# Kernel tuning notes

Hardware: AMD Instinct MI355X
Metric: run time of the kernel (lower is better)

The kernel has to match this reference:

```python
import jax, jax.numpy as jnp
import numpy as np

N_NODES = 100000

def gcn_conv(x, edge_index, W, b, n_nodes):
    # GCNConv: out = D^{-1/2} (A + I) D^{-1/2} X W + b  (self-loops added)
    src, dst = edge_index[0], edge_index[1]
    loops = jnp.arange(n_nodes, dtype=edge_index.dtype)
    src = jnp.concatenate([src, loops])
    dst = jnp.concatenate([dst, loops])
    deg = jax.ops.segment_sum(jnp.ones_like(dst, dtype=x.dtype), dst, num_segments=n_nodes)
    dinv = jnp.where(deg > 0, jax.lax.rsqrt(deg), 0.0)
    norm = dinv[src] * dinv[dst]  # [E+N]
    h = x @ W  # transform first (small d), then gather/scatter
    msgs = h[src] * norm[:, None]
    out = jax.ops.segment_sum(msgs, dst, num_segments=n_nodes)
    return out + b


def setup_inputs() -> dict:
    key = jax.random.key(0)
    k1, k2, k3, k4, k5, k6 = jax.random.split(key, 6)
    x = jax.random.normal(k1, (N_NODES, 3), dtype=jnp.float32)
    edge_index = jax.random.randint(k2, (2, 2400000), 0, N_NODES, dtype=jnp.int64)
    # Glorot-style init for GCNConv linear weights; zero bias matches PyG default
    W1 = jax.random.normal(k3, (3, 16), dtype=jnp.float32) * (1.0 / np.sqrt(3))
    b1 = jnp.zeros((16,), dtype=jnp.float32)
    W2 = jax.random.normal(k4, (16, 32), dtype=jnp.float32) * (1.0 / np.sqrt(16))
    b2 = jnp.zeros((32,), dtype=jnp.float32)
    return {"x": x, "edge_index": edge_index, "W1": W1, "b1": b1, "W2": W2, "b2": b2}


def reference(x, edge_index, W1, b1, W2, b2):
    n = x.shape[0]
    h = gcn_conv(x, edge_index, W1, b1, n)
    h = jax.nn.relu(h)
    h = gcn_conv(h, edge_index, W2, b2, n)
    # batch is all zeros in the original forward -> single-graph mean pool
    return jnp.mean(h, axis=0, keepdims=True)  # [1, 32]
```

## Files before the change

kernel.cpp:

```cpp
#include <hip/hip_runtime.h>

typedef unsigned int uint;
typedef unsigned long long ull;


#define MAXB  256
#define CAP   16384u
#define BINB  512
#define CHUNK 4096
#define AFS   2048.0f
#define AFB   16384
#define AFM   0x1FFFFFu
#define PADN  131072

__global__ void __launch_bounds__(BINB)
bin2_kernel(const int* __restrict__ srcI, const int* __restrict__ dstI,
            uint* __restrict__ curDg, uint* __restrict__ curSg,
            uint* __restrict__ bufD, uint* __restrict__ bufS, int E) {
    __shared__ uint cntD[MAXB], scanD[MAXB], baseD[MAXB];
    __shared__ uint cntS[MAXB], scanS[MAXB], baseS[MAXB];
    __shared__ uint stageD[CHUNK];
    __shared__ uint stageS[CHUNK];
    const int tid = threadIdx.x;
    const int e0 = blockIdx.x * CHUNK;
    const int nE = min(CHUNK, E - e0);
    const int my0 = tid * 8;
    const int myc = max(0, min(8, nE - my0));
    if (tid < MAXB) cntD[tid] = 0u; else cntS[tid - MAXB] = 0u;

    uint d8[8], s8[8], rD[8], rS[8];
    if (myc == 8) {
        int4 ka = ((const int4*)(dstI + e0))[tid * 2];
        int4 kb = ((const int4*)(dstI + e0))[tid * 2 + 1];
        int4 oa = ((const int4*)(srcI + e0))[tid * 2];
        int4 ob = ((const int4*)(srcI + e0))[tid * 2 + 1];
        d8[0] = ka.x; d8[1] = ka.y; d8[2] = ka.z; d8[3] = ka.w;
        d8[4] = kb.x; d8[5] = kb.y; d8[6] = kb.z; d8[7] = kb.w;
        s8[0] = oa.x; s8[1] = oa.y; s8[2] = oa.z; s8[3] = oa.w;
        s8[4] = ob.x; s8[5] = ob.y; s8[6] = ob.z; s8[7] = ob.w;
    } else {
        for (int r = 0; r < myc; ++r) {
            d8[r] = (uint)dstI[e0 + my0 + r];
            s8[r] = (uint)srcI[e0 + my0 + r];
        }
    }
    __syncthreads();
    for (int r = 0; r < myc; ++r) {
        rD[r] = atomicAdd(&cntD[d8[r] >> 9], 1u);
        rS[r] = atomicAdd(&cntS[s8[r] >> 9], 1u);
    }
    __syncthreads();
    const int half = tid >> 8;
    const int li = tid & 255;
    uint* cn = half ? cntS : cntD;
    uint* sc = half ? scanS : scanD;
    sc[li] = cn[li];
    __syncthreads();
    for (int d = 1; d < MAXB; d <<= 1) {
        uint t = (li >= d) ? sc[li - d] : 0u;
        __syncthreads();
        sc[li] += t;
        __syncthreads();
    }
    {
        uint* cur = half ? curSg : curDg;
        uint* bs = half ? baseS : baseD;
        bs[li] = (uint)li * CAP + (cn[li] ? atomicAdd(&cur[li * 16], cn[li]) : 0u);
    }
    __syncthreads();
    for (int r = 0; r < myc; ++r) {
        uint bD = d8[r] >> 9;
        stageD[(scanD[bD] - cntD[bD]) + rD[r]] = ((d8[r] & 511u) << 17) | s8[r];
        uint bS = s8[r] >> 9;
        stageS[(scanS[bS] - cntS[bS]) + rS[r]] = ((s8[r] & 511u) << 17) | d8[r];
    }
    __syncthreads();
    const int wave = tid >> 6, lane = tid & 63;
    if (wave < 4) {
        for (int b = wave; b < MAXB; b += 4) {
            uint s0 = scanD[b] - cntD[b], c = cntD[b], gb = baseD[b];
            uint lim = (uint)(b + 1) * CAP;
            for (uint i = lane; i < c; i += 64u) {
                uint gp = gb + i;
                if (gp < lim) bufD[gp] = stageD[s0 + i];
            }
        }
    } else {
        for (int b = wave - 4; b < MAXB; b += 4) {
            uint s0 = scanS[b] - cntS[b], c = cntS[b], gb = baseS[b];
            uint lim = (uint)(b + 1) * CAP;
            for (uint i = lane; i < c; i += 64u) {
                uint gp = gb + i;
                if (gp < lim) bufS[gp] = stageS[s0 + i];
            }
        }
    }
}

__global__ void __launch_bounds__(1024)
degnode_kernel(const uint* __restrict__ buf, const uint* __restrict__ curD,
               const float* __restrict__ x, uint* __restrict__ degg,
               float* __restrict__ dinv, float4* __restrict__ xd4, int n) {
    __shared__ uint dg[512];
    const int tid = threadIdx.x;
    const int b = blockIdx.x;
    const uint base = (uint)b * CAP;
    const uint c = min(curD[b * 16], CAP);
    if (tid < 512) dg[tid] = 0u;
    __syncthreads();
    for (uint i0 = (uint)tid * 8u; i0 < c; i0 += 8192u) {
        uint cnt8 = min(8u, c - i0);
        uint en[8];
        if (cnt8 == 8u) {
            uint4 a = ((const uint4*)(buf + base + i0))[0];
            uint4 bb = ((const uint4*)(buf + base + i0))[1];
            en[0] = a.x; en[1] = a.y; en[2] = a.z; en[3] = a.w;
            en[4] = bb.x; en[5] = bb.y; en[6] = bb.z; en[7] = bb.w;
        } else {
            for (uint r = 0; r < cnt8; ++r) en[r] = buf[base + i0 + r];
        }
        for (uint r = 0; r < cnt8; ++r) atomicAdd(&dg[en[r] >> 17], 1u);
    }
    __syncthreads();
    if (tid < 512) {
        int node = (b << 9) + tid;
        if (node < n) {
            uint d = dg[tid];
            degg[node] = d;
            float di = rsqrtf((float)(d + 1u));
            dinv[node] = di;
            xd4[node] = make_float4(x[3 * node] * di, x[3 * node + 1] * di,
                                    x[3 * node + 2] * di, di);
        }
    }
}

__global__ void __launch_bounds__(1024)
aggqT_kernel(const uint* __restrict__ bufD, const uint* __restrict__ curD,
             const uint* __restrict__ bufS, const uint* __restrict__ curS,
             const uint* __restrict__ degg, const float* __restrict__ dinv,
             const float4* __restrict__ xd4, const float* __restrict__ W1,
             const float* __restrict__ b1, float* __restrict__ T, int n) {
    __shared__ ull acc[512];
    __shared__ float gl[512];
    __shared__ float taccs[16];
    const int tid = threadIdx.x;
    const int b = blockIdx.x;
    const uint base = (uint)b * CAP;
    const uint cD = min(curD[b * 16], CAP);
    const uint cS = min(curS[b * 16], CAP);
    if (tid < 512) { acc[tid] = 0ull; gl[tid] = 0.0f; }
    if (tid < 16) taccs[tid] = 0.0f;
    __syncthreads();
    for (uint i0 = (uint)tid * 8u; i0 < cS; i0 += 8192u) {
        uint cnt8 = min(8u, cS - i0);
        uint en[8];
        if (cnt8 == 8u) {
            uint4 a = ((const uint4*)(bufS + base + i0))[0];
            uint4 bb = ((const uint4*)(bufS + base + i0))[1];
            en[0] = a.x; en[1] = a.y; en[2] = a.z; en[3] = a.w;
            en[4] = bb.x; en[5] = bb.y; en[6] = bb.z; en[7] = bb.w;
        } else {
            for (uint r = 0; r < cnt8; ++r) en[r] = bufS[base + i0 + r];
            for (uint r = cnt8; r < 8u; ++r) en[r] = en[0];
        }
        float dv[8];
#pragma unroll
        for (int r = 0; r < 8; ++r) dv[r] = dinv[en[r] & 0x1FFFFu];
#pragma unroll
        for (uint r = 0; r < 8u; ++r)
            if (r < cnt8) atomicAdd(&gl[en[r] >> 17], dv[r]);
    }
    for (uint i0 = (uint)tid * 8u; i0 < cD; i0 += 8192u) {
        uint cnt8 = min(8u, cD - i0);
        uint en[8];
        if (cnt8 == 8u) {
            uint4 a = ((const uint4*)(bufD + base + i0))[0];
            uint4 bb = ((const uint4*)(bufD + base + i0))[1];
            en[0] = a.x; en[1] = a.y; en[2] = a.z; en[3] = a.w;
            en[4] = bb.x; en[5] = bb.y; en[6] = bb.z; en[7] = bb.w;
        } else {
            for (uint r = 0; r < cnt8; ++r) en[r] = bufD[base + i0 + r];
            for (uint r = cnt8; r < 8u; ++r) en[r] = en[0];
        }
        float4 gv[8];
#pragma unroll
        for (int r = 0; r < 8; ++r) gv[r] = xd4[en[r] & 0x1FFFFu];
#pragma unroll
        for (uint r = 0; r < 8u; ++r) {
            if (r < cnt8) {
                uint dl = en[r] >> 17;
                ull f0 = (ull)(uint)((int)rintf(gv[r].x * AFS) + AFB);
                ull f1 = (ull)(uint)((int)rintf(gv[r].y * AFS) + AFB);
                ull f2 = (ull)(uint)((int)rintf(gv[r].z * AFS) + AFB);
                atomicAdd(&acc[dl], f0 | (f1 << 21) | (f2 << 42));
            }
        }
    }
    __syncthreads();
    float sq[16];
#pragma unroll
    for (int k = 0; k < 16; ++k) sq[k] = 0.0f;
    if (tid < 512) {
        int node = (b << 9) + tid;
        if (node < n) {
            ull v = acc[tid];
            int ub = (int)(degg[node] * (uint)AFB);
            float4 sv = xd4[node];
            float di = sv.w;
            const float isc = 1.0f / AFS;
            float av = (float)((int)(uint)(v & AFM) - ub) * isc + sv.x;
            float bv = (float)((int)(uint)((v >> 21) & AFM) - ub) * isc + sv.y;
            float cv = (float)((int)(uint)((v >> 42) & AFM) - ub) * isc + sv.z;
            float w = gl[tid] + di;
#pragma unroll
            for (int k = 0; k < 16; ++k) {
                float h = di * (av * W1[k] + bv * W1[16 + k] + cv * W1[32 + k]) + b1[k];
                h = fmaxf(h, 0.0f);
                sq[k] = w * (di * h);
            }
        }
    }
#pragma unroll
    for (int k = 0; k < 16; ++k) {
        float v2 = sq[k];
        for (int off = 32; off > 0; off >>= 1) v2 += __shfl_down(v2, off, 64);
        if ((tid & 63) == 0) atomicAdd(&taccs[k], v2);
    }
    __syncthreads();
    if (tid < 16 && taccs[tid] != 0.0f) atomicAdd(&T[tid], taccs[tid]);
}

__global__ void out_kernel(const float* __restrict__ T, const float* __restrict__ W2,
                           const float* __restrict__ b2, float* __restrict__ out, float invN) {
    int j = threadIdx.x;
    float s = 0.0f;
#pragma unroll
    for (int k = 0; k < 16; ++k) s += T[k] * W2[k * 32 + j];
    out[j] = b2[j] + invN * s;
}

extern "C" void kernel_launch(void* const* d_in, const int* in_sizes, int n_in,
                              void* d_out, int out_size, void* d_ws, size_t ws_size,
                              hipStream_t stream) {
    const float* x   = (const float*)d_in[0];
    const int*   ei  = (const int*)d_in[1];
    const float* W1  = (const float*)d_in[2];
    const float* b1  = (const float*)d_in[3];
    const float* W2  = (const float*)d_in[4];
    const float* b2  = (const float*)d_in[5];
    float* out = (float*)d_out;

    const int n = in_sizes[0] / 3;
    const int E = in_sizes[1] / 2;
    const int* src = ei;
    const int* dst = ei + E;

    char* p = (char*)d_ws;
    float* T    = (float*)p;    p += 64;
    uint*  curD = (uint*)p;     p += MAXB * 16 * 4;
    uint*  curS = (uint*)p;     p += MAXB * 16 * 4;
    size_t zbytes = (size_t)(p - (char*)d_ws);
    uint*  degg  = (uint*)p;    p += (size_t)n * 4;
    float* dinv  = (float*)p;   p += (size_t)n * 4;
    uint*  bufD  = (uint*)p;    p += (size_t)MAXB * CAP * 4;
    uint*  bufS  = (uint*)p;    p += (size_t)MAXB * CAP * 4;
    p = (char*)(((size_t)p + 31) & ~(size_t)31);
    float4* xd4  = (float4*)p;  p += (size_t)PADN * 16;

    const int nb = (n + 511) >> 9;

    hipMemsetAsync(d_ws, 0, zbytes, stream);
    bin2_kernel<<<(E + CHUNK - 1) / CHUNK, BINB, 0, stream>>>(src, dst, curD, curS, bufD, bufS, E);
    degnode_kernel<<<nb, 1024, 0, stream>>>(bufD, curD, x, degg, dinv, xd4, n);
    aggqT_kernel<<<nb, 1024, 0, stream>>>(bufD, curD, bufS, curS, degg, dinv, xd4, W1, b1, T, n);
    out_kernel<<<1, 32, 0, stream>>>(T, W2, b2, out, 1.0f / (float)n);
}
```

Measured before the change: 144.6 us.

## Flatten bin scatter, split aggregation sweeps across half-blocks, fuse output via last-block

```diff
diff --git a/kernel.cpp b/kernel.cpp
--- a/kernel.cpp
+++ b/kernel.cpp
@@ -2,6 +2,7 @@
 
 typedef unsigned int uint;
 typedef unsigned long long ull;
+typedef unsigned char uchar;
 
 
 #define MAXB  256
@@ -17,10 +18,12 @@
 bin2_kernel(const int* __restrict__ srcI, const int* __restrict__ dstI,
             uint* __restrict__ curDg, uint* __restrict__ curSg,
             uint* __restrict__ bufD, uint* __restrict__ bufS, int E) {
-    __shared__ uint cntD[MAXB], scanD[MAXB], baseD[MAXB];
-    __shared__ uint cntS[MAXB], scanS[MAXB], baseS[MAXB];
+    __shared__ uint cntD[MAXB], scanD[MAXB], deltaD[MAXB];
+    __shared__ uint cntS[MAXB], scanS[MAXB], deltaS[MAXB];
     __shared__ uint stageD[CHUNK];
     __shared__ uint stageS[CHUNK];
+    __shared__ uchar stBD[CHUNK];
+    __shared__ uchar stBS[CHUNK];
     const int tid = threadIdx.x;
     const int e0 = blockIdx.x * CHUNK;
     const int nE = min(CHUNK, E - e0);
@@ -64,35 +67,32 @@
     }
     {
         uint* cur = half ? curSg : curDg;
-        uint* bs = half ? baseS : baseD;
-        bs[li] = (uint)li * CAP + (cn[li] ? atomicAdd(&cur[li * 16], cn[li]) : 0u);
+        uint* dl = half ? deltaS : deltaD;
+        uint gbase = (uint)li * CAP + (cn[li] ? atomicAdd(&cur[li * 16], cn[li]) : 0u);
+        dl[li] = gbase - (sc[li] - cn[li]);
     }
     __syncthreads();
     for (int r = 0; r < myc; ++r) {
         uint bD = d8[r] >> 9;
-        stageD[(scanD[bD] - cntD[bD]) + rD[r]] = ((d8[r] & 511u) << 17) | s8[r];
+        uint pD = (scanD[bD] - cntD[bD]) + rD[r];
+        stageD[pD] = ((d8[r] & 511u) << 17) | s8[r];
+        stBD[pD] = (uchar)bD;
         uint bS = s8[r] >> 9;
-        stageS[(scanS[bS] - cntS[bS]) + rS[r]] = ((s8[r] & 511u) << 17) | d8[r];
-    }
-    __syncthreads();
-    const int wave = tid >> 6, lane = tid & 63;
-    if (wave < 4) {
-        for (int b = wave; b < MAXB; b += 4) {
-            uint s0 = scanD[b] - cntD[b], c = cntD[b], gb = baseD[b];
-            uint lim = (uint)(b + 1) * CAP;
-            for (uint i = lane; i < c; i += 64u) {
-                uint gp = gb + i;
-                if (gp < lim) bufD[gp] = stageD[s0 + i];
-            }
-        }
-    } else {
-        for (int b = wave - 4; b < MAXB; b += 4) {
-            uint s0 = scanS[b] - cntS[b], c = cntS[b], gb = baseS[b];
-            uint lim = (uint)(b + 1) * CAP;
-            for (uint i = lane; i < c; i += 64u) {
-                uint gp = gb + i;
-                if (gp < lim) bufS[gp] = stageS[s0 + i];
-            }
+        uint pS = (scanS[bS] - cntS[bS]) + rS[r];
+        stageS[pS] = ((s8[r] & 511u) << 17) | d8[r];
+        stBS[pS] = (uchar)bS;
+    }
+    __syncthreads();
+#pragma unroll
+    for (int r = 0; r < 8; ++r) {
+        int i = r * BINB + tid;
+        if (i < nE) {
+            uint b = stBD[i];
+            uint gp = deltaD[b] + (uint)i;
+            if (gp < (b + 1u) * CAP) bufD[gp] = stageD[i];
+            uint b2 = stBS[i];
+            uint gp2 = deltaS[b2] + (uint)i;
+            if (gp2 < (b2 + 1u) * CAP) bufS[gp2] = stageS[i];
         }
     }
 }
@@ -140,10 +140,14 @@
              const uint* __restrict__ bufS, const uint* __restrict__ curS,
              const uint* __restrict__ degg, const float* __restrict__ dinv,
              const float4* __restrict__ xd4, const float* __restrict__ W1,
-             const float* __restrict__ b1, float* __restrict__ T, int n) {
+             const float* __restrict__ b1, const float* __restrict__ W2,
+             const float* __restrict__ b2, float* __restrict__ T,
+             uint* __restrict__ doneCtr, float* __restrict__ out, int n) {
     __shared__ ull acc[512];
     __shared__ float gl[512];
     __shared__ float taccs[16];
+    __shared__ float tval[16];
+    __shared__ int lastB;
     const int tid = threadIdx.x;
     const int b = blockIdx.x;
     const uint base = (uint)b * CAP;
@@ -152,48 +156,53 @@
     if (tid < 512) { acc[tid] = 0ull; gl[tid] = 0.0f; }
     if (tid < 16) taccs[tid] = 0.0f;
     __syncthreads();
-    for (uint i0 = (uint)tid * 8u; i0 < cS; i0 += 8192u) {
-        uint cnt8 = min(8u, cS - i0);
-        uint en[8];
-        if (cnt8 == 8u) {
-            uint4 a = ((const uint4*)(bufS + base + i0))[0];
-            uint4 bb = ((const uint4*)(bufS + base + i0))[1];
-            en[0] = a.x; en[1] = a.y; en[2] = a.z; en[3] = a.w;
-            en[4] = bb.x; en[5] = bb.y; en[6] = bb.z; en[7] = bb.w;
-        } else {
-            for (uint r = 0; r < cnt8; ++r) en[r] = bufS[base + i0 + r];
-            for (uint r = cnt8; r < 8u; ++r) en[r] = en[0];
-        }
-        float dv[8];
-#pragma unroll
-        for (int r = 0; r < 8; ++r) dv[r] = dinv[en[r] & 0x1FFFFu];
-#pragma unroll
-        for (uint r = 0; r < 8u; ++r)
-            if (r < cnt8) atomicAdd(&gl[en[r] >> 17], dv[r]);
-    }
-    for (uint i0 = (uint)tid * 8u; i0 < cD; i0 += 8192u) {
-        uint cnt8 = min(8u, cD - i0);
-        uint en[8];
-        if (cnt8 == 8u) {
-            uint4 a = ((const uint4*)(bufD + base + i0))[0];
-            uint4 bb = ((const uint4*)(bufD + base + i0))[1];
-            en[0] = a.x; en[1] = a.y; en[2] = a.z; en[3] = a.w;
-            en[4] = bb.x; en[5] = bb.y; en[6] = bb.z; en[7] = bb.w;
-        } else {
-            for (uint r = 0; r < cnt8; ++r) en[r] = bufD[base + i0 + r];
-            for (uint r = cnt8; r < 8u; ++r) en[r] = en[0];
-        }
-        float4 gv[8];
-#pragma unroll
-        for (int r = 0; r < 8; ++r) gv[r] = xd4[en[r] & 0x1FFFFu];
-#pragma unroll
-        for (uint r = 0; r < 8u; ++r) {
-            if (r < cnt8) {
-                uint dl = en[r] >> 17;
-                ull f0 = (ull)(uint)((int)rintf(gv[r].x * AFS) + AFB);
-                ull f1 = (ull)(uint)((int)rintf(gv[r].y * AFS) + AFB);
-                ull f2 = (ull)(uint)((int)rintf(gv[r].z * AFS) + AFB);
-                atomicAdd(&acc[dl], f0 | (f1 << 21) | (f2 << 42));
+    const int sweep = tid >> 9;
+    const uint ht = (uint)(tid & 511);
+    if (sweep == 0) {
+        for (uint i0 = ht * 8u; i0 < cS; i0 += 4096u) {
+            uint cnt8 = min(8u, cS - i0);
+            uint en[8];
+            if (cnt8 == 8u) {
+                uint4 a = ((const uint4*)(bufS + base + i0))[0];
+                uint4 bb = ((const uint4*)(bufS + base + i0))[1];
+                en[0] = a.x; en[1] = a.y; en[2] = a.z; en[3] = a.w;
+                en[4] = bb.x; en[5] = bb.y; en[6] = bb.z; en[7] = bb.w;
+            } else {
+                for (uint r = 0; r < cnt8; ++r) en[r] = bufS[base + i0 + r];
+                for (uint r = cnt8; r < 8u; ++r) en[r] = en[0];
+            }
+            float dv[8];
+#pragma unroll
+            for (int r = 0; r < 8; ++r) dv[r] = dinv[en[r] & 0x1FFFFu];
+#pragma unroll
+            for (uint r = 0; r < 8u; ++r)
+                if (r < cnt8) atomicAdd(&gl[en[r] >> 17], dv[r]);
+        }
+    } else {
+        for (uint i0 = ht * 8u; i0 < cD; i0 += 4096u) {
+            uint cnt8 = min(8u, cD - i0);
+            uint en[8];
+            if (cnt8 == 8u) {
+                uint4 a = ((const uint4*)(bufD + base + i0))[0];
+                uint4 bb = ((const uint4*)(bufD + base + i0))[1];
+                en[0] = a.x; en[1] = a.y; en[2] = a.z; en[3] = a.w;
+                en[4] = bb.x; en[5] = bb.y; en[6] = bb.z; en[7] = bb.w;
+            } else {
+                for (uint r = 0; r < cnt8; ++r) en[r] = bufD[base + i0 + r];
+                for (uint r = cnt8; r < 8u; ++r) en[r] = en[0];
+            }
+            float4 gv[8];
+#pragma unroll
+            for (int r = 0; r < 8; ++r) gv[r] = xd4[en[r] & 0x1FFFFu];
+#pragma unroll
+            for (uint r = 0; r < 8u; ++r) {
+                if (r < cnt8) {
+                    uint dl = en[r] >> 17;
+                    ull f0 = (ull)(uint)((int)rintf(gv[r].x * AFS) + AFB);
+                    ull f1 = (ull)(uint)((int)rintf(gv[r].y * AFS) + AFB);
+                    ull f2 = (ull)(uint)((int)rintf(gv[r].z * AFS) + AFB);
+                    atomicAdd(&acc[dl], f0 | (f1 << 21) | (f2 << 42));
+                }
             }
         }
     }
@@ -229,15 +238,23 @@
     }
     __syncthreads();
     if (tid < 16 && taccs[tid] != 0.0f) atomicAdd(&T[tid], taccs[tid]);
-}
-
-__global__ void out_kernel(const float* __restrict__ T, const float* __restrict__ W2,
-                           const float* __restrict__ b2, float* __restrict__ out, float invN) {
-    int j = threadIdx.x;
-    float s = 0.0f;
-#pragma unroll
-    for (int k = 0; k < 16; ++k) s += T[k] * W2[k * 32 + j];
-    out[j] = b2[j] + invN * s;
+    __syncthreads();
+    if (tid == 0) {
+        __threadfence();
+        uint t = atomicAdd(doneCtr, 1u);
+        lastB = (t == (uint)(gridDim.x - 1)) ? 1 : 0;
+    }
+    __syncthreads();
+    if (lastB) {
+        if (tid < 16) tval[tid] = atomicAdd(&T[tid], 0.0f);
+        __syncthreads();
+        if (tid < 32) {
+            float s2 = 0.0f;
+#pragma unroll
+            for (int k = 0; k < 16; ++k) s2 += tval[k] * W2[k * 32 + tid];
+            out[tid] = b2[tid] + (1.0f / (float)n) * s2;
+        }
+    }
 }
 
 extern "C" void kernel_launch(void* const* d_in, const int* in_sizes, int n_in,
@@ -258,6 +275,7 @@
 
     char* p = (char*)d_ws;
     float* T    = (float*)p;    p += 64;
+    uint*  done = (uint*)p;     p += 64;
     uint*  curD = (uint*)p;     p += MAXB * 16 * 4;
     uint*  curS = (uint*)p;     p += MAXB * 16 * 4;
     size_t zbytes = (size_t)(p - (char*)d_ws);
@@ -273,6 +291,6 @@
     hipMemsetAsync(d_ws, 0, zbytes, stream);
     bin2_kernel<<<(E + CHUNK - 1) / CHUNK, BINB, 0, stream>>>(src, dst, curD, curS, bufD, bufS, E);
     degnode_kernel<<<nb, 1024, 0, stream>>>(bufD, curD, x, degg, dinv, xd4, n);
-    aggqT_kernel<<<nb, 1024, 0, stream>>>(bufD, curD, bufS, curS, degg, dinv, xd4, W1, b1, T, n);
-    out_kernel<<<1, 32, 0, stream>>>(T, W2, b2, out, 1.0f / (float)n);
-}
+    aggqT_kernel<<<nb, 1024, 0, stream>>>(bufD, curD, bufS, curS, degg, dinv, xd4,
+                                          W1, b1, W2, b2, T, done, out, n);
+}
```

Measured after the change: 135.4 us. 1.07x faster.
